# Performance work log

Measured on AMD Instinct MI355X. Metric: run time of the kernel, lower is better.

Reference implementation:

```python
import jax, jax.numpy as jnp
import numpy as np

N_NODES = 100000
N_EDGES = 3200000
IN_DIM = 64


def gcn_conv(x, edge_index, edge_weight, W, b, num_nodes):
    """PyG GCNConv: h = x @ W; add self-loops (w=1); symmetric norm; scatter-add; + bias."""
    src = edge_index[0]
    dst = edge_index[1]
    loop = jnp.arange(num_nodes)
    src_a = jnp.concatenate([src, loop])
    dst_a = jnp.concatenate([dst, loop])
    w_a = jnp.concatenate([edge_weight, jnp.ones((num_nodes,), dtype=edge_weight.dtype)])
    # degree at target nodes (weighted, incl. self-loops)
    deg = jax.ops.segment_sum(w_a, dst_a, num_segments=num_nodes)
    dinv = jnp.where(deg > 0, jax.lax.rsqrt(deg), 0.0)
    norm = dinv[src_a] * w_a * dinv[dst_a]  # [E+N]
    h = x @ W  # [N, out] - transform before propagate (cheaper: out_dim small)
    msg = h[src_a] * norm[:, None]  # [E+N, out]
    out = jax.ops.segment_sum(msg, dst_a, num_segments=num_nodes)
    return out + b


def setup_inputs() -> dict:
    key = jax.random.key(0)
    ks = jax.random.split(key, 9)
    x = jax.random.normal(ks[0], (N_NODES, IN_DIM), dtype=jnp.float32)
    edge_index = jax.random.randint(ks[1], (2, N_EDGES), 0, N_NODES, dtype=jnp.int64)
    edge_weight = jax.random.uniform(ks[2], (N_EDGES,), dtype=jnp.float32)
    s1 = 1.0 / np.sqrt(IN_DIM)
    W1 = jax.random.uniform(ks[3], (IN_DIM, 16), jnp.float32, -s1, s1)
    b1 = jnp.zeros((16,), jnp.float32)
    s2 = 1.0 / np.sqrt(16)
    W2 = jax.random.uniform(ks[4], (16, 2), jnp.float32, -s2, s2)
    b2 = jnp.zeros((2,), jnp.float32)
    s3 = 1.0 / np.sqrt(2)
    lin_w = jax.random.uniform(ks[5], (2, 1), jnp.float32, -s3, s3)
    lin_b = jax.random.uniform(ks[6], (1,), jnp.float32, -s3, s3)
    return {"x": x, "edge_index": edge_index, "edge_weight": edge_weight,
            "W1": W1, "b1": b1, "W2": W2, "b2": b2, "lin_w": lin_w, "lin_b": lin_b}


def reference(x, edge_index, edge_weight, W1, b1, W2, b2, lin_w, lin_b):
    h = gcn_conv(x, edge_index, edge_weight, W1, b1, N_NODES)
    h = jax.nn.relu(h)
    # F.dropout in eval mode = identity (deterministic reference)
    x2 = gcn_conv(h, edge_index, edge_weight, W2, b2, N_NODES)  # [N, 2]
    out = jax.nn.relu(x2)
    out = jax.nn.sigmoid(out @ lin_w + lin_b)  # [N, 1]
    return (out, x2)
```

## Files before the change

kernel.cpp:

```cpp
#include <hip/hip_runtime.h>
#include <math.h>

#define N_NODES 100000
#define N_EDGES 3200000
#define LO_BITS 7
#define NPB 128
#define NB  ((N_NODES + NPB - 1) / NPB)
#define PART_B 512
#define PART_T 1024
#define CPB (N_EDGES / PART_B)
#define BCAP 5120
#define CMAX 10

typedef unsigned long long u64;
typedef unsigned int u32;
typedef unsigned short u16;

static __device__ inline u16 f2bf(float f) {
    u32 u = __float_as_uint(f);
    return (u16)((u + 0x7FFF + ((u >> 16) & 1)) >> 16);
}
static __device__ inline float bf2f(u16 h) {
    return __uint_as_float((u32)h << 16);
}

static __device__ inline int wave_iscan(int x, int lane) {
#pragma unroll
    for (int off = 1; off < 64; off <<= 1) {
        int u = __shfl_up(x, off, 64);
        if (lane >= off) x += u;
    }
    return x;
}


__global__ void __launch_bounds__(PART_T) hist_k(const int* __restrict__ dst,
                                                 int* __restrict__ hist_mat) {
    __shared__ int h[NB];
    for (int t = threadIdx.x; t < NB; t += blockDim.x) h[t] = 0;
    __syncthreads();
    int base = blockIdx.x * CPB;
    for (int it = 0; it < (CPB + PART_T - 1) / PART_T; it++) {
        int e = base + it * PART_T + threadIdx.x;
        if (e < base + CPB) {
            int d = dst[e];
            atomicAdd(&h[d >> LO_BITS], 1);
        }
    }
    __syncthreads();
    for (int t = threadIdx.x; t < NB; t += blockDim.x)
        hist_mat[blockIdx.x * NB + t] = h[t];
}

__global__ void __launch_bounds__(PART_B) colscan_k(const int* __restrict__ hist_mat,
                                                    int* __restrict__ hist_excl,
                                                    int* __restrict__ tot) {
    __shared__ int wsum[PART_B / 64];
    int bin = blockIdx.x, t = threadIdx.x;
    int lane = t & 63, w = t >> 6;
    int v = hist_mat[t * NB + bin];
    int x = wave_iscan(v, lane);
    if (lane == 63) wsum[w] = x;
    __syncthreads();
    int base = 0;
#pragma unroll
    for (int i = 0; i < PART_B / 64; i++)
        if (i < w) base += wsum[i];
    hist_excl[t * NB + bin] = base + x - v;
    if (t == PART_B - 1) tot[bin] = base + x;
}

__global__ void base_k(const int* __restrict__ tot, int* __restrict__ bbase) {
    __shared__ int wsum[16];
    int t = threadIdx.x, lane = t & 63, w = t >> 6;
    int v = (t < NB) ? tot[t] : 0;
    int x = wave_iscan(v, lane);
    if (lane == 63) wsum[w] = x;
    __syncthreads();
    int base = 0;
#pragma unroll
    for (int i = 0; i < 16; i++)
        if (i < w) base += wsum[i];
    if (t < NB) bbase[t] = base + x - v;
    if (t == 0) bbase[NB] = N_EDGES;
}

__global__ void __launch_bounds__(PART_T) part_k(
        const int* __restrict__ src, const int* __restrict__ dst,
        const float* __restrict__ w, const int* __restrict__ hist_mat,
        const int* __restrict__ hist_excl,
        const int* __restrict__ bbase, u64* __restrict__ ebuf) {
    __shared__ u64 sorted[CPB];
    __shared__ int cur[NB];
    __shared__ int gofs[NB];
    __shared__ int swsum[PART_T / 64];
    int t = threadIdx.x;
    int lane = t & 63, wv = t >> 6;
    int base = blockIdx.x * CPB;
    int rawc = (t < NB) ? hist_mat[blockIdx.x * NB + t] : 0;
    int x = wave_iscan(rawc, lane);
    if (lane == 63) swsum[wv] = x;
    __syncthreads();
    int bs = 0;
#pragma unroll
    for (int i = 0; i < PART_T / 64; i++)
        if (i < wv) bs += swsum[i];
    if (t < NB) {
        int lscan = bs + x - rawc;
        cur[t] = lscan;
        gofs[t] = bbase[t] + hist_excl[blockIdx.x * NB + t] - lscan;
    }
    __syncthreads();
#pragma unroll
    for (int it = 0; it < (CPB + PART_T - 1) / PART_T; it++) {
        int e = base + it * PART_T + t;
        if (e < base + CPB) {
            int d = dst[e];
            int sv = __builtin_nontemporal_load(&src[e]);
            u32 wvv = __float_as_uint(__builtin_nontemporal_load(&w[e]));
            int pos = atomicAdd(&cur[d >> LO_BITS], 1);
            sorted[pos] = ((u64)(u32)sv << 47) | ((u64)(u32)d << 30) | (u64)(wvv >> 2);
        }
    }
    __syncthreads();
    for (int p = t; p < CPB; p += PART_T) {
        u64 pk = sorted[p];
        int sv = (int)(pk >> 47);
        int d  = (int)((pk >> 30) & 0x1FFFF);
        u32 wvv = ((u32)pk & 0x3FFFFFFF) << 2;
        u32 hi = ((u32)sv << LO_BITS) | (u32)(d & (NPB - 1));
        ebuf[gofs[d >> LO_BITS] + p] = ((u64)hi << 32) | (u64)wvv;
    }
}

__global__ void __launch_bounds__(512) csr_deg_k(
        const u64* __restrict__ ebuf, const int* __restrict__ bbase,
        int* __restrict__ row_ptr, float* __restrict__ dinv,
        u64* __restrict__ pedge) {
    __shared__ u64 staged[BCAP];
    __shared__ int   cnt[NPB];
    __shared__ float wsum[NPB];
    __shared__ int   cur[NPB];
    __shared__ int   cw[2];
    int b = blockIdx.x, t = threadIdx.x;
    if (t < NPB) { cnt[t] = 0; wsum[t] = 0.0f; }
    __syncthreads();
    int j0 = bbase[b], j1 = bbase[b + 1];
    u64 pe[CMAX];
    int nit = 0;
#pragma unroll
    for (int it = 0; it < CMAX; it++) {
        int j = j0 + it * 512 + t;
        if (j < j1) {
            u64 e = ebuf[j];
            pe[it] = e;
            int lo = (int)((u32)(e >> 32) & (NPB - 1));
            atomicAdd(&cnt[lo], 1);
            atomicAdd(&wsum[lo], __uint_as_float((u32)e));
            nit = it + 1;
        }
    }
    for (int j = j0 + 512 * CMAX + t; j < j1; j += 512) {
        u64 e = ebuf[j];
        int lo = (int)((u32)(e >> 32) & (NPB - 1));
        atomicAdd(&cnt[lo], 1);
        atomicAdd(&wsum[lo], __uint_as_float((u32)e));
    }
    __syncthreads();
    int lane = t & 63;
    int v = (t < NPB) ? cnt[t] : 0;
    int x = wave_iscan(v, lane);
    if (t < NPB && lane == 63) cw[t >> 6] = x;
    __syncthreads();
    if (t < NPB) {
        int incl = x + ((t >= 64) ? cw[0] : 0);
        int excl = incl - v;
        cur[t] = excl;
        int node = b * NPB + t;
        if (node < N_NODES) {
            row_ptr[node] = j0 + excl;
            dinv[node] = rsqrtf(1.0f + wsum[t]);
        }
    }
    if (b == NB - 1 && t == 0) row_ptr[N_NODES] = N_EDGES;
    __syncthreads();
#pragma unroll
    for (int it = 0; it < CMAX; it++) {
        if (it < nit) {
            u64 e = pe[it];
            u32 hi = (u32)(e >> 32);
            int lo = (int)(hi & (NPB - 1));
            int p = atomicAdd(&cur[lo], 1);
            u64 val = ((u64)(hi >> LO_BITS) << 32) | (u64)(u32)e;
            if (p < BCAP) staged[p] = val;
            else pedge[j0 + p] = val;
        }
    }
    for (int j = j0 + 512 * CMAX + t; j < j1; j += 512) {
        u64 e = ebuf[j];
        u32 hi = (u32)(e >> 32);
        int lo = (int)(hi & (NPB - 1));
        int p = atomicAdd(&cur[lo], 1);
        u64 val = ((u64)(hi >> LO_BITS) << 32) | (u64)(u32)e;
        if (p < BCAP) staged[p] = val;
        else pedge[j0 + p] = val;
    }
    __syncthreads();
    int nbe = j1 - j0;
    int lim = nbe < BCAP ? nbe : BCAP;
    for (int p = t; p < lim; p += 512) pedge[j0 + p] = staged[p];
}


__global__ void __launch_bounds__(256) gemm1(
        const float* __restrict__ x, const float* __restrict__ W1,
        const float* __restrict__ dinv, u16* __restrict__ g1b) {
    __shared__ float sW[64 * 16];
    __shared__ float xs[16][68];
    for (int t = threadIdx.x; t < 64 * 16; t += blockDim.x) sW[t] = W1[t];
    int nbase = blockIdx.x * 16;
    {
        int q = threadIdx.x;
        const float4 v = ((const float4*)(x + (size_t)nbase * 64))[q];
        int n = q >> 4, f4 = q & 15;
        xs[n][f4 * 4 + 0] = v.x;
        xs[n][f4 * 4 + 1] = v.y;
        xs[n][f4 * 4 + 2] = v.z;
        xs[n][f4 * 4 + 3] = v.w;
    }
    __syncthreads();
    int n = threadIdx.x >> 4, c = threadIdx.x & 15;
    int node = nbase + n;
    float acc = 0.0f;
#pragma unroll
    for (int k = 0; k < 64; k++) acc += xs[n][k] * sW[k * 16 + c];
    g1b[node * 16 + c] = f2bf(acc * dinv[node]);
}

__global__ void gather1(const int* __restrict__ row_ptr, const u64* __restrict__ pedge,
                        const float* __restrict__ dinv, const u32* __restrict__ g1w,
                        const float* __restrict__ b1, const float* __restrict__ W2,
                        float* __restrict__ y2) {
    int gid = blockIdx.x * blockDim.x + threadIdx.x;
    int node = gid >> 6;
    if (node >= N_NODES) return;
    int lane = threadIdx.x & 63;
    int c2 = lane & 7;
    int eg = lane >> 3;
    int j0 = row_ptr[node], j1 = row_ptr[node + 1];
    float a0 = 0.0f, a1 = 0.0f;
    for (int base = j0; base < j1; base += 64) {
        int idx = base + lane;
        u64 se = (idx < j1) ? __builtin_nontemporal_load(&pedge[idx]) : 0ULL;
        for (int k = 0; k < 8; k++) {
            if (base + k * 8 >= j1) break;
            u64 pe = __shfl(se, k * 8 + eg, 64);
            int s = (int)(pe >> 32);
            float wr = __uint_as_float((u32)pe);
            u32 g2 = g1w[s * 8 + c2];
            a0 += bf2f((u16)g2) * wr;
            a1 += bf2f((u16)(g2 >> 16)) * wr;
        }
    }
    a0 += __shfl_xor(a0, 8, 64);  a1 += __shfl_xor(a1, 8, 64);
    a0 += __shfl_xor(a0, 16, 64); a1 += __shfl_xor(a1, 16, 64);
    a0 += __shfl_xor(a0, 32, 64); a1 += __shfl_xor(a1, 32, 64);
    u32 gs = g1w[node * 8 + c2];
    a0 += bf2f((u16)gs);
    a1 += bf2f((u16)(gs >> 16));
    float di = dinv[node];
    int c0 = c2 * 2, c1 = c0 + 1;
    float v0 = a0 * di + b1[c0]; v0 = v0 > 0.0f ? v0 : 0.0f;
    float v1 = a1 * di + b1[c1]; v1 = v1 > 0.0f ? v1 : 0.0f;
    float p0 = v0 * W2[c0 * 2]     + v1 * W2[c1 * 2];
    float p1 = v0 * W2[c0 * 2 + 1] + v1 * W2[c1 * 2 + 1];
    p0 += __shfl_xor(p0, 1, 64); p1 += __shfl_xor(p1, 1, 64);
    p0 += __shfl_xor(p0, 2, 64); p1 += __shfl_xor(p1, 2, 64);
    p0 += __shfl_xor(p0, 4, 64); p1 += __shfl_xor(p1, 4, 64);
    if (lane == 0) {
        y2[node * 2]     = p0 * di;
        y2[node * 2 + 1] = p1 * di;
    }
}

__global__ void gather2(const int* __restrict__ row_ptr, const u64* __restrict__ pedge,
                        const float* __restrict__ dinv, const float* __restrict__ y2,
                        const float* __restrict__ b2, const float* __restrict__ lin_w,
                        const float* __restrict__ lin_b, float* __restrict__ out) {
    int gid = blockIdx.x * blockDim.x + threadIdx.x;
    int i = gid >> 6;
    if (i >= N_NODES) return;
    int lane = threadIdx.x & 63;
    int k = lane & 1;
    int el = lane >> 1;
    int j0 = row_ptr[i], j1 = row_ptr[i + 1];
    float a = 0.0f;
    for (int base = j0; base < j1; base += 64) {
        int idx = base + lane;
        u64 se = (idx < j1) ? __builtin_nontemporal_load(&pedge[idx]) : 0ULL;
        for (int k2 = 0; k2 < 2; k2++) {
            if (base + k2 * 32 >= j1) break;
            u64 pe = __shfl(se, k2 * 32 + el, 64);
            int s = (int)(pe >> 32);
            float wr = __uint_as_float((u32)pe);
            a += y2[s * 2 + k] * wr;
        }
    }
    a += __shfl_xor(a, 2, 64);
    a += __shfl_xor(a, 4, 64);
    a += __shfl_xor(a, 8, 64);
    a += __shfl_xor(a, 16, 64);
    a += __shfl_xor(a, 32, 64);
    float ao = __shfl_xor(a, 1, 64);
    if (lane == 0) {
        float di = dinv[i];
        float y0 = y2[i * 2], y1 = y2[i * 2 + 1];
        float x20 = (a + y0) * di + b2[0];
        float x21 = (ao + y1) * di + b2[1];
        out[N_NODES + i * 2]     = x20;
        out[N_NODES + i * 2 + 1] = x21;
        float r0 = x20 > 0.0f ? x20 : 0.0f;
        float r1 = x21 > 0.0f ? x21 : 0.0f;
        float z = r0 * lin_w[0] + r1 * lin_w[1] + lin_b[0];
        out[i] = 1.0f / (1.0f + expf(-z));
    }
}

extern "C" void kernel_launch(void* const* d_in, const int* in_sizes, int n_in,
                              void* d_out, int out_size, void* d_ws, size_t ws_size,
                              hipStream_t stream) {
    const float* x     = (const float*)d_in[0];
    const int*   ei    = (const int*)d_in[1];
    const float* ew    = (const float*)d_in[2];
    const float* W1    = (const float*)d_in[3];
    const float* b1    = (const float*)d_in[4];
    const float* W2    = (const float*)d_in[5];
    const float* b2    = (const float*)d_in[6];
    const float* lin_w = (const float*)d_in[7];
    const float* lin_b = (const float*)d_in[8];
    float* out = (float*)d_out;

    const int* src = ei;
    const int* dst = ei + N_EDGES;

    char* w8 = (char*)d_ws;
    size_t off = 0;
    auto take = [&](size_t bytes) { char* p = w8 + off; off += (bytes + 15) & ~((size_t)15); return (void*)p; };
    u64*   ebuf      = (u64*)  take((size_t)N_EDGES * 8);
    u64*   pedge     = (u64*)  take((size_t)N_EDGES * 8);
    int*   hist_mat  = (int*)  take((size_t)PART_B * NB * 4);
    int*   hist_excl = (int*)  take((size_t)PART_B * NB * 4);
    int*   tot       = (int*)  take((size_t)NB * 4);
    int*   bbase     = (int*)  take((size_t)(NB + 1) * 4);
    int*   row_ptr   = (int*)  take((size_t)(N_NODES + 1) * 4);
    float* dinv      = (float*)take((size_t)N_NODES * 4);
    u16*   g1b       = (u16*)ebuf;
    u32*   g1w       = (u32*)ebuf;
    float* y2        = (float*)ebuf + (size_t)8 * N_NODES;

    const int B = 256;

    hist_k<<<PART_B, PART_T, 0, stream>>>(dst, hist_mat);
    colscan_k<<<NB, PART_B, 0, stream>>>(hist_mat, hist_excl, tot);
    base_k<<<1, 1024, 0, stream>>>(tot, bbase);
    part_k<<<PART_B, PART_T, 0, stream>>>(src, dst, ew, hist_mat, hist_excl, bbase, ebuf);

    csr_deg_k<<<NB, 512, 0, stream>>>(ebuf, bbase, row_ptr, dinv, pedge);

    gemm1<<<N_NODES / 16, B, 0, stream>>>(x, W1, dinv, g1b);
    gather1<<<(64 * N_NODES + B - 1) / B, B, 0, stream>>>(row_ptr, pedge, dinv, g1w, b1, W2, y2);

    gather2<<<(64 * N_NODES + B - 1) / B, B, 0, stream>>>(row_ptr, pedge, dinv, y2, b2,
                                                         lin_w, lin_b, out);
}
```

Measured before the change: 255.1 us.

## Replace per-node CSR build with bucket-level shared-memory atomic aggregation

Drops the second-level sort that built a full CSR (row_ptr and a per-node edge array). The bucketed edge buffer is consumed directly. Each block of 128 destination nodes walks its bucket's edges and accumulates messages into shared memory with float atomics, for both GCN layers and the degree pass. This removes one full pass that wrote 25.6 MB of edges, plus the sort atomics. The cost is many LDS atomic adds per edge (16 in layer 1), possible contention on hot nodes, and a summation order that is no longer deterministic.

Measured after the change: 576.6 us. 2.26x slower.

```diff
diff --git a/kernel.cpp b/kernel.cpp
--- a/kernel.cpp
+++ b/kernel.cpp
@@ -9,8 +9,6 @@
 #define PART_B 512
 #define PART_T 1024
 #define CPB (N_EDGES / PART_B)
-#define BCAP 5120
-#define CMAX 10
 
 typedef unsigned long long u64;
 typedef unsigned int u32;
@@ -133,82 +131,24 @@
     }
 }
 
-__global__ void __launch_bounds__(512) csr_deg_k(
+__global__ void __launch_bounds__(512) deg_k(
         const u64* __restrict__ ebuf, const int* __restrict__ bbase,
-        int* __restrict__ row_ptr, float* __restrict__ dinv,
-        u64* __restrict__ pedge) {
-    __shared__ u64 staged[BCAP];
-    __shared__ int   cnt[NPB];
+        float* __restrict__ dinv) {
     __shared__ float wsum[NPB];
-    __shared__ int   cur[NPB];
-    __shared__ int   cw[2];
     int b = blockIdx.x, t = threadIdx.x;
-    if (t < NPB) { cnt[t] = 0; wsum[t] = 0.0f; }
+    if (t < NPB) wsum[t] = 0.0f;
     __syncthreads();
     int j0 = bbase[b], j1 = bbase[b + 1];
-    u64 pe[CMAX];
-    int nit = 0;
-#pragma unroll
-    for (int it = 0; it < CMAX; it++) {
-        int j = j0 + it * 512 + t;
-        if (j < j1) {
-            u64 e = ebuf[j];
-            pe[it] = e;
-            int lo = (int)((u32)(e >> 32) & (NPB - 1));
-            atomicAdd(&cnt[lo], 1);
-            atomicAdd(&wsum[lo], __uint_as_float((u32)e));
-            nit = it + 1;
-        }
-    }
-    for (int j = j0 + 512 * CMAX + t; j < j1; j += 512) {
+    for (int j = j0 + t; j < j1; j += 512) {
         u64 e = ebuf[j];
-        int lo = (int)((u32)(e >> 32) & (NPB - 1));
-        atomicAdd(&cnt[lo], 1);
-        atomicAdd(&wsum[lo], __uint_as_float((u32)e));
-    }
-    __syncthreads();
-    int lane = t & 63;
-    int v = (t < NPB) ? cnt[t] : 0;
-    int x = wave_iscan(v, lane);
-    if (t < NPB && lane == 63) cw[t >> 6] = x;
+        int n = (int)((u32)(e >> 32) & (NPB - 1));
+        atomicAdd(&wsum[n], __uint_as_float((u32)e));
+    }
     __syncthreads();
     if (t < NPB) {
-        int incl = x + ((t >= 64) ? cw[0] : 0);
-        int excl = incl - v;
-        cur[t] = excl;
         int node = b * NPB + t;
-        if (node < N_NODES) {
-            row_ptr[node] = j0 + excl;
-            dinv[node] = rsqrtf(1.0f + wsum[t]);
-        }
-    }
-    if (b == NB - 1 && t == 0) row_ptr[N_NODES] = N_EDGES;
-    __syncthreads();
-#pragma unroll
-    for (int it = 0; it < CMAX; it++) {
-        if (it < nit) {
-            u64 e = pe[it];
-            u32 hi = (u32)(e >> 32);
-            int lo = (int)(hi & (NPB - 1));
-            int p = atomicAdd(&cur[lo], 1);
-            u64 val = ((u64)(hi >> LO_BITS) << 32) | (u64)(u32)e;
-            if (p < BCAP) staged[p] = val;
-            else pedge[j0 + p] = val;
-        }
-    }
-    for (int j = j0 + 512 * CMAX + t; j < j1; j += 512) {
-        u64 e = ebuf[j];
-        u32 hi = (u32)(e >> 32);
-        int lo = (int)(hi & (NPB - 1));
-        int p = atomicAdd(&cur[lo], 1);
-        u64 val = ((u64)(hi >> LO_BITS) << 32) | (u64)(u32)e;
-        if (p < BCAP) staged[p] = val;
-        else pedge[j0 + p] = val;
-    }
-    __syncthreads();
-    int nbe = j1 - j0;
-    int lim = nbe < BCAP ? nbe : BCAP;
-    for (int p = t; p < lim; p += 512) pedge[j0 + p] = staged[p];
+        if (node < N_NODES) dinv[node] = rsqrtf(1.0f + wsum[t]);
+    }
 }
 
 
@@ -237,92 +177,107 @@
     g1b[node * 16 + c] = f2bf(acc * dinv[node]);
 }
 
-__global__ void gather1(const int* __restrict__ row_ptr, const u64* __restrict__ pedge,
-                        const float* __restrict__ dinv, const u32* __restrict__ g1w,
-                        const float* __restrict__ b1, const float* __restrict__ W2,
-                        float* __restrict__ y2) {
-    int gid = blockIdx.x * blockDim.x + threadIdx.x;
-    int node = gid >> 6;
-    if (node >= N_NODES) return;
-    int lane = threadIdx.x & 63;
-    int c2 = lane & 7;
-    int eg = lane >> 3;
-    int j0 = row_ptr[node], j1 = row_ptr[node + 1];
-    float a0 = 0.0f, a1 = 0.0f;
-    for (int base = j0; base < j1; base += 64) {
-        int idx = base + lane;
-        u64 se = (idx < j1) ? __builtin_nontemporal_load(&pedge[idx]) : 0ULL;
-        for (int k = 0; k < 8; k++) {
-            if (base + k * 8 >= j1) break;
-            u64 pe = __shfl(se, k * 8 + eg, 64);
-            int s = (int)(pe >> 32);
-            float wr = __uint_as_float((u32)pe);
-            u32 g2 = g1w[s * 8 + c2];
-            a0 += bf2f((u16)g2) * wr;
-            a1 += bf2f((u16)(g2 >> 16)) * wr;
-        }
-    }
-    a0 += __shfl_xor(a0, 8, 64);  a1 += __shfl_xor(a1, 8, 64);
-    a0 += __shfl_xor(a0, 16, 64); a1 += __shfl_xor(a1, 16, 64);
-    a0 += __shfl_xor(a0, 32, 64); a1 += __shfl_xor(a1, 32, 64);
-    u32 gs = g1w[node * 8 + c2];
-    a0 += bf2f((u16)gs);
-    a1 += bf2f((u16)(gs >> 16));
-    float di = dinv[node];
-    int c0 = c2 * 2, c1 = c0 + 1;
-    float v0 = a0 * di + b1[c0]; v0 = v0 > 0.0f ? v0 : 0.0f;
-    float v1 = a1 * di + b1[c1]; v1 = v1 > 0.0f ? v1 : 0.0f;
-    float p0 = v0 * W2[c0 * 2]     + v1 * W2[c1 * 2];
-    float p1 = v0 * W2[c0 * 2 + 1] + v1 * W2[c1 * 2 + 1];
-    p0 += __shfl_xor(p0, 1, 64); p1 += __shfl_xor(p1, 1, 64);
-    p0 += __shfl_xor(p0, 2, 64); p1 += __shfl_xor(p1, 2, 64);
-    p0 += __shfl_xor(p0, 4, 64); p1 += __shfl_xor(p1, 4, 64);
-    if (lane == 0) {
-        y2[node * 2]     = p0 * di;
-        y2[node * 2 + 1] = p1 * di;
-    }
-}
-
-__global__ void gather2(const int* __restrict__ row_ptr, const u64* __restrict__ pedge,
-                        const float* __restrict__ dinv, const float* __restrict__ y2,
-                        const float* __restrict__ b2, const float* __restrict__ lin_w,
-                        const float* __restrict__ lin_b, float* __restrict__ out) {
-    int gid = blockIdx.x * blockDim.x + threadIdx.x;
-    int i = gid >> 6;
-    if (i >= N_NODES) return;
-    int lane = threadIdx.x & 63;
-    int k = lane & 1;
-    int el = lane >> 1;
-    int j0 = row_ptr[i], j1 = row_ptr[i + 1];
-    float a = 0.0f;
-    for (int base = j0; base < j1; base += 64) {
-        int idx = base + lane;
-        u64 se = (idx < j1) ? __builtin_nontemporal_load(&pedge[idx]) : 0ULL;
-        for (int k2 = 0; k2 < 2; k2++) {
-            if (base + k2 * 32 >= j1) break;
-            u64 pe = __shfl(se, k2 * 32 + el, 64);
-            int s = (int)(pe >> 32);
-            float wr = __uint_as_float((u32)pe);
-            a += y2[s * 2 + k] * wr;
-        }
-    }
-    a += __shfl_xor(a, 2, 64);
-    a += __shfl_xor(a, 4, 64);
-    a += __shfl_xor(a, 8, 64);
-    a += __shfl_xor(a, 16, 64);
-    a += __shfl_xor(a, 32, 64);
-    float ao = __shfl_xor(a, 1, 64);
-    if (lane == 0) {
-        float di = dinv[i];
-        float y0 = y2[i * 2], y1 = y2[i * 2 + 1];
-        float x20 = (a + y0) * di + b2[0];
-        float x21 = (ao + y1) * di + b2[1];
-        out[N_NODES + i * 2]     = x20;
-        out[N_NODES + i * 2 + 1] = x21;
-        float r0 = x20 > 0.0f ? x20 : 0.0f;
-        float r1 = x21 > 0.0f ? x21 : 0.0f;
-        float z = r0 * lin_w[0] + r1 * lin_w[1] + lin_b[0];
-        out[i] = 1.0f / (1.0f + expf(-z));
+__global__ void __launch_bounds__(512) g1_k(
+        const u64* __restrict__ ebuf, const int* __restrict__ bbase,
+        const float* __restrict__ dinv, const u32* __restrict__ g1w,
+        const float* __restrict__ b1, const float* __restrict__ W2,
+        float* __restrict__ y2) {
+    __shared__ float acc[NPB * 17];
+    __shared__ float y2a[NPB * 2];
+    int b = blockIdx.x, t = threadIdx.x;
+    for (int q = t; q < NPB * 17; q += 512) acc[q] = 0.0f;
+    if (t < NPB * 2) y2a[t] = 0.0f;
+    __syncthreads();
+    int j0 = bbase[b], j1 = bbase[b + 1];
+    for (int j = j0 + t; j < j1; j += 512) {
+        u64 e = ebuf[j];
+        u32 hi = (u32)(e >> 32);
+        int n = (int)(hi & (NPB - 1));
+        int s = (int)(hi >> LO_BITS);
+        float wr = __uint_as_float((u32)e);
+        const uint4* rp = (const uint4*)(g1w + (size_t)s * 8);
+        uint4 r0 = rp[0];
+        uint4 r1 = rp[1];
+        float* ap = acc + n * 17;
+        atomicAdd(ap + 0,  bf2f((u16)r0.x) * wr);
+        atomicAdd(ap + 1,  bf2f((u16)(r0.x >> 16)) * wr);
+        atomicAdd(ap + 2,  bf2f((u16)r0.y) * wr);
+        atomicAdd(ap + 3,  bf2f((u16)(r0.y >> 16)) * wr);
+        atomicAdd(ap + 4,  bf2f((u16)r0.z) * wr);
+        atomicAdd(ap + 5,  bf2f((u16)(r0.z >> 16)) * wr);
+        atomicAdd(ap + 6,  bf2f((u16)r0.w) * wr);
+        atomicAdd(ap + 7,  bf2f((u16)(r0.w >> 16)) * wr);
+        atomicAdd(ap + 8,  bf2f((u16)r1.x) * wr);
+        atomicAdd(ap + 9,  bf2f((u16)(r1.x >> 16)) * wr);
+        atomicAdd(ap + 10, bf2f((u16)r1.y) * wr);
+        atomicAdd(ap + 11, bf2f((u16)(r1.y >> 16)) * wr);
+        atomicAdd(ap + 12, bf2f((u16)r1.z) * wr);
+        atomicAdd(ap + 13, bf2f((u16)(r1.z >> 16)) * wr);
+        atomicAdd(ap + 14, bf2f((u16)r1.w) * wr);
+        atomicAdd(ap + 15, bf2f((u16)(r1.w >> 16)) * wr);
+    }
+    __syncthreads();
+#pragma unroll
+    for (int it = 0; it < 4; it++) {
+        int id = t + it * 512;
+        int n = id >> 4, f = id & 15;
+        int node = b * NPB + n;
+        if (node < N_NODES) {
+            u32 gs = g1w[node * 8 + (f >> 1)];
+            float self = bf2f((u16)((f & 1) ? (gs >> 16) : (gs & 0xFFFF)));
+            float di = dinv[node];
+            float v = (acc[n * 17 + f] + self) * di + b1[f];
+            v = v > 0.0f ? v : 0.0f;
+            atomicAdd(&y2a[n * 2],     v * W2[2 * f]);
+            atomicAdd(&y2a[n * 2 + 1], v * W2[2 * f + 1]);
+        }
+    }
+    __syncthreads();
+    if (t < NPB) {
+        int node = b * NPB + t;
+        if (node < N_NODES) {
+            float di = dinv[node];
+            y2[node * 2]     = y2a[t * 2] * di;
+            y2[node * 2 + 1] = y2a[t * 2 + 1] * di;
+        }
+    }
+}
+
+__global__ void __launch_bounds__(512) g2_k(
+        const u64* __restrict__ ebuf, const int* __restrict__ bbase,
+        const float* __restrict__ dinv, const float* __restrict__ y2,
+        const float* __restrict__ b2, const float* __restrict__ lin_w,
+        const float* __restrict__ lin_b, float* __restrict__ out) {
+    __shared__ float a2[NPB * 2];
+    int b = blockIdx.x, t = threadIdx.x;
+    if (t < NPB * 2) a2[t] = 0.0f;
+    __syncthreads();
+    int j0 = bbase[b], j1 = bbase[b + 1];
+    for (int j = j0 + t; j < j1; j += 512) {
+        u64 e = ebuf[j];
+        u32 hi = (u32)(e >> 32);
+        int n = (int)(hi & (NPB - 1));
+        int s = (int)(hi >> LO_BITS);
+        float wr = __uint_as_float((u32)e);
+        float2 yv = *(const float2*)(y2 + (size_t)s * 2);
+        atomicAdd(&a2[n * 2],     yv.x * wr);
+        atomicAdd(&a2[n * 2 + 1], yv.y * wr);
+    }
+    __syncthreads();
+    if (t < NPB) {
+        int node = b * NPB + t;
+        if (node < N_NODES) {
+            float di = dinv[node];
+            float y0 = y2[node * 2], y1 = y2[node * 2 + 1];
+            float x20 = (a2[t * 2]     + y0) * di + b2[0];
+            float x21 = (a2[t * 2 + 1] + y1) * di + b2[1];
+            out[N_NODES + node * 2]     = x20;
+            out[N_NODES + node * 2 + 1] = x21;
+            float r0 = x20 > 0.0f ? x20 : 0.0f;
+            float r1 = x21 > 0.0f ? x21 : 0.0f;
+            float z = r0 * lin_w[0] + r1 * lin_w[1] + lin_b[0];
+            out[node] = 1.0f / (1.0f + expf(-z));
+        }
     }
 }
 
@@ -347,29 +302,24 @@
     size_t off = 0;
     auto take = [&](size_t bytes) { char* p = w8 + off; off += (bytes + 15) & ~((size_t)15); return (void*)p; };
     u64*   ebuf      = (u64*)  take((size_t)N_EDGES * 8);
-    u64*   pedge     = (u64*)  take((size_t)N_EDGES * 8);
     int*   hist_mat  = (int*)  take((size_t)PART_B * NB * 4);
     int*   hist_excl = (int*)  take((size_t)PART_B * NB * 4);
     int*   tot       = (int*)  take((size_t)NB * 4);
     int*   bbase     = (int*)  take((size_t)(NB + 1) * 4);
-    int*   row_ptr   = (int*)  take((size_t)(N_NODES + 1) * 4);
     float* dinv      = (float*)take((size_t)N_NODES * 4);
-    u16*   g1b       = (u16*)ebuf;
-    u32*   g1w       = (u32*)ebuf;
-    float* y2        = (float*)ebuf + (size_t)8 * N_NODES;
-
-    const int B = 256;
+    u16*   g1b       = (u16*)  take((size_t)N_NODES * 16 * 2);
+    float* y2        = (float*)take((size_t)N_NODES * 2 * 4);
+    u32*   g1w       = (u32*)g1b;
 
     hist_k<<<PART_B, PART_T, 0, stream>>>(dst, hist_mat);
     colscan_k<<<NB, PART_B, 0, stream>>>(hist_mat, hist_excl, tot);
     base_k<<<1, 1024, 0, stream>>>(tot, bbase);
     part_k<<<PART_B, PART_T, 0, stream>>>(src, dst, ew, hist_mat, hist_excl, bbase, ebuf);
 
-    csr_deg_k<<<NB, 512, 0, stream>>>(ebuf, bbase, row_ptr, dinv, pedge);
-
-    gemm1<<<N_NODES / 16, B, 0, stream>>>(x, W1, dinv, g1b);
-    gather1<<<(64 * N_NODES + B - 1) / B, B, 0, stream>>>(row_ptr, pedge, dinv, g1w, b1, W2, y2);
-
-    gather2<<<(64 * N_NODES + B - 1) / B, B, 0, stream>>>(row_ptr, pedge, dinv, y2, b2,
-                                                         lin_w, lin_b, out);
-}
+    deg_k<<<NB, 512, 0, stream>>>(ebuf, bbase, dinv);
+
+    gemm1<<<N_NODES / 16, 256, 0, stream>>>(x, W1, dinv, g1b);
+    g1_k<<<NB, 512, 0, stream>>>(ebuf, bbase, dinv, g1w, b1, W2, y2);
+
+    g2_k<<<NB, 512, 0, stream>>>(ebuf, bbase, dinv, y2, b2, lin_w, lin_b, out);
+}
```

## Use sub-wave thread groups per node in both CSR gather kernels

Applied to the files above, without the earlier changes.

Gather1 now assigns 4 threads per node, each loading 4 bf16 features with a uint2 load and processing two edges per iteration. Gather2 uses 2 threads per node that split the edges and load both y2 components as a float2. Previously each node took a full 64-lane wavefront, which left most lanes idle at the average degree of about 32 edges. The new mapping launches far fewer threads and cuts shuffle reductions, but each thread walks its edge list serially, so load imbalance grows and each wave's edge reads are less coalesced.

Measured after the change: 274.8 us. 7.7% more time.

```diff
diff --git a/kernel.cpp b/kernel.cpp
--- a/kernel.cpp
+++ b/kernel.cpp
@@ -237,86 +237,87 @@
     g1b[node * 16 + c] = f2bf(acc * dinv[node]);
 }
 
-__global__ void gather1(const int* __restrict__ row_ptr, const u64* __restrict__ pedge,
-                        const float* __restrict__ dinv, const u32* __restrict__ g1w,
-                        const float* __restrict__ b1, const float* __restrict__ W2,
-                        float* __restrict__ y2) {
+__global__ void __launch_bounds__(256) gather1(
+        const int* __restrict__ row_ptr, const u64* __restrict__ pedge,
+        const float* __restrict__ dinv, const u32* __restrict__ g1w,
+        const float* __restrict__ b1, const float* __restrict__ W2,
+        float* __restrict__ y2) {
     int gid = blockIdx.x * blockDim.x + threadIdx.x;
-    int node = gid >> 6;
+    int node = gid >> 2;
     if (node >= N_NODES) return;
-    int lane = threadIdx.x & 63;
-    int c2 = lane & 7;
-    int eg = lane >> 3;
+    int q = gid & 3;
     int j0 = row_ptr[node], j1 = row_ptr[node + 1];
-    float a0 = 0.0f, a1 = 0.0f;
-    for (int base = j0; base < j1; base += 64) {
-        int idx = base + lane;
-        u64 se = (idx < j1) ? __builtin_nontemporal_load(&pedge[idx]) : 0ULL;
-        for (int k = 0; k < 8; k++) {
-            if (base + k * 8 >= j1) break;
-            u64 pe = __shfl(se, k * 8 + eg, 64);
-            int s = (int)(pe >> 32);
-            float wr = __uint_as_float((u32)pe);
-            u32 g2 = g1w[s * 8 + c2];
-            a0 += bf2f((u16)g2) * wr;
-            a1 += bf2f((u16)(g2 >> 16)) * wr;
-        }
-    }
-    a0 += __shfl_xor(a0, 8, 64);  a1 += __shfl_xor(a1, 8, 64);
-    a0 += __shfl_xor(a0, 16, 64); a1 += __shfl_xor(a1, 16, 64);
-    a0 += __shfl_xor(a0, 32, 64); a1 += __shfl_xor(a1, 32, 64);
-    u32 gs = g1w[node * 8 + c2];
-    a0 += bf2f((u16)gs);
-    a1 += bf2f((u16)(gs >> 16));
+    float a0 = 0.0f, a1 = 0.0f, a2 = 0.0f, a3 = 0.0f;
+    int j = j0;
+    for (; j + 2 <= j1; j += 2) {
+        u64 pe0 = __builtin_nontemporal_load(&pedge[j]);
+        u64 pe1 = __builtin_nontemporal_load(&pedge[j + 1]);
+        int s0 = (int)(pe0 >> 32);
+        int s1 = (int)(pe1 >> 32);
+        uint2 ga = *(const uint2*)(g1w + (size_t)s0 * 8 + q * 2);
+        uint2 gb = *(const uint2*)(g1w + (size_t)s1 * 8 + q * 2);
+        float w0 = __uint_as_float((u32)pe0);
+        float w1 = __uint_as_float((u32)pe1);
+        a0 += bf2f((u16)ga.x) * w0;  a1 += bf2f((u16)(ga.x >> 16)) * w0;
+        a2 += bf2f((u16)ga.y) * w0;  a3 += bf2f((u16)(ga.y >> 16)) * w0;
+        a0 += bf2f((u16)gb.x) * w1;  a1 += bf2f((u16)(gb.x >> 16)) * w1;
+        a2 += bf2f((u16)gb.y) * w1;  a3 += bf2f((u16)(gb.y >> 16)) * w1;
+    }
+    if (j < j1) {
+        u64 pe0 = __builtin_nontemporal_load(&pedge[j]);
+        int s0 = (int)(pe0 >> 32);
+        uint2 ga = *(const uint2*)(g1w + (size_t)s0 * 8 + q * 2);
+        float w0 = __uint_as_float((u32)pe0);
+        a0 += bf2f((u16)ga.x) * w0;  a1 += bf2f((u16)(ga.x >> 16)) * w0;
+        a2 += bf2f((u16)ga.y) * w0;  a3 += bf2f((u16)(ga.y >> 16)) * w0;
+    }
+    uint2 gs = *(const uint2*)(g1w + (size_t)node * 8 + q * 2);
+    a0 += bf2f((u16)gs.x);  a1 += bf2f((u16)(gs.x >> 16));
+    a2 += bf2f((u16)gs.y);  a3 += bf2f((u16)(gs.y >> 16));
     float di = dinv[node];
-    int c0 = c2 * 2, c1 = c0 + 1;
-    float v0 = a0 * di + b1[c0]; v0 = v0 > 0.0f ? v0 : 0.0f;
-    float v1 = a1 * di + b1[c1]; v1 = v1 > 0.0f ? v1 : 0.0f;
-    float p0 = v0 * W2[c0 * 2]     + v1 * W2[c1 * 2];
-    float p1 = v0 * W2[c0 * 2 + 1] + v1 * W2[c1 * 2 + 1];
-    p0 += __shfl_xor(p0, 1, 64); p1 += __shfl_xor(p1, 1, 64);
-    p0 += __shfl_xor(p0, 2, 64); p1 += __shfl_xor(p1, 2, 64);
-    p0 += __shfl_xor(p0, 4, 64); p1 += __shfl_xor(p1, 4, 64);
-    if (lane == 0) {
+    int f0 = q * 4;
+    float v0 = a0 * di + b1[f0];     v0 = v0 > 0.0f ? v0 : 0.0f;
+    float v1 = a1 * di + b1[f0 + 1]; v1 = v1 > 0.0f ? v1 : 0.0f;
+    float v2 = a2 * di + b1[f0 + 2]; v2 = v2 > 0.0f ? v2 : 0.0f;
+    float v3 = a3 * di + b1[f0 + 3]; v3 = v3 > 0.0f ? v3 : 0.0f;
+    float p0 = v0 * W2[2 * f0]     + v1 * W2[2 * f0 + 2]
+             + v2 * W2[2 * f0 + 4] + v3 * W2[2 * f0 + 6];
+    float p1 = v0 * W2[2 * f0 + 1] + v1 * W2[2 * f0 + 3]
+             + v2 * W2[2 * f0 + 5] + v3 * W2[2 * f0 + 7];
+    p0 += __shfl_xor(p0, 1, 64);  p1 += __shfl_xor(p1, 1, 64);
+    p0 += __shfl_xor(p0, 2, 64);  p1 += __shfl_xor(p1, 2, 64);
+    if (q == 0) {
         y2[node * 2]     = p0 * di;
         y2[node * 2 + 1] = p1 * di;
     }
 }
 
-__global__ void gather2(const int* __restrict__ row_ptr, const u64* __restrict__ pedge,
-                        const float* __restrict__ dinv, const float* __restrict__ y2,
-                        const float* __restrict__ b2, const float* __restrict__ lin_w,
-                        const float* __restrict__ lin_b, float* __restrict__ out) {
+__global__ void __launch_bounds__(256) gather2(
+        const int* __restrict__ row_ptr, const u64* __restrict__ pedge,
+        const float* __restrict__ dinv, const float* __restrict__ y2,
+        const float* __restrict__ b2, const float* __restrict__ lin_w,
+        const float* __restrict__ lin_b, float* __restrict__ out) {
     int gid = blockIdx.x * blockDim.x + threadIdx.x;
-    int i = gid >> 6;
+    int i = gid >> 1;
     if (i >= N_NODES) return;
-    int lane = threadIdx.x & 63;
-    int k = lane & 1;
-    int el = lane >> 1;
+    int h = gid & 1;
     int j0 = row_ptr[i], j1 = row_ptr[i + 1];
-    float a = 0.0f;
-    for (int base = j0; base < j1; base += 64) {
-        int idx = base + lane;
-        u64 se = (idx < j1) ? __builtin_nontemporal_load(&pedge[idx]) : 0ULL;
-        for (int k2 = 0; k2 < 2; k2++) {
-            if (base + k2 * 32 >= j1) break;
-            u64 pe = __shfl(se, k2 * 32 + el, 64);
-            int s = (int)(pe >> 32);
-            float wr = __uint_as_float((u32)pe);
-            a += y2[s * 2 + k] * wr;
-        }
-    }
-    a += __shfl_xor(a, 2, 64);
-    a += __shfl_xor(a, 4, 64);
-    a += __shfl_xor(a, 8, 64);
-    a += __shfl_xor(a, 16, 64);
-    a += __shfl_xor(a, 32, 64);
-    float ao = __shfl_xor(a, 1, 64);
-    if (lane == 0) {
+    float a0 = 0.0f, a1 = 0.0f;
+    for (int j = j0 + h; j < j1; j += 2) {
+        u64 pe = __builtin_nontemporal_load(&pedge[j]);
+        int s = (int)(pe >> 32);
+        float wr = __uint_as_float((u32)pe);
+        float2 yv = *(const float2*)(y2 + (size_t)s * 2);
+        a0 += yv.x * wr;
+        a1 += yv.y * wr;
+    }
+    a0 += __shfl_xor(a0, 1, 64);
+    a1 += __shfl_xor(a1, 1, 64);
+    if (h == 0) {
         float di = dinv[i];
         float y0 = y2[i * 2], y1 = y2[i * 2 + 1];
-        float x20 = (a + y0) * di + b2[0];
-        float x21 = (ao + y1) * di + b2[1];
+        float x20 = (a0 + y0) * di + b2[0];
+        float x21 = (a1 + y1) * di + b2[1];
         out[N_NODES + i * 2]     = x20;
         out[N_NODES + i * 2 + 1] = x21;
         float r0 = x20 > 0.0f ? x20 : 0.0f;
@@ -368,8 +369,8 @@
     csr_deg_k<<<NB, 512, 0, stream>>>(ebuf, bbase, row_ptr, dinv, pedge);
 
     gemm1<<<N_NODES / 16, B, 0, stream>>>(x, W1, dinv, g1b);
-    gather1<<<(64 * N_NODES + B - 1) / B, B, 0, stream>>>(row_ptr, pedge, dinv, g1w, b1, W2, y2);
-
-    gather2<<<(64 * N_NODES + B - 1) / B, B, 0, stream>>>(row_ptr, pedge, dinv, y2, b2,
-                                                         lin_w, lin_b, out);
-}
+    gather1<<<(4 * N_NODES + B - 1) / B, B, 0, stream>>>(row_ptr, pedge, dinv, g1w, b1, W2, y2);
+
+    gather2<<<(2 * N_NODES + B - 1) / B, B, 0, stream>>>(row_ptr, pedge, dinv, y2, b2,
+                                                        lin_w, lin_b, out);
+}
```
